# Performance work log

Hardware: AMD Instinct MI355X
Metric: run time of the kernel (lower is better)

The kernel has to match this reference:

```python
import jax, jax.numpy as jnp
import numpy as np

N = 2048  # device_num
K = 32    # neighbors per device


def setup_inputs() -> dict:
    key = jax.random.key(0)
    k1, k2, k3 = jax.random.split(key, 3)
    dynamic_re = jax.random.uniform(k1, (N, N), dtype=jnp.float32)
    static_re = jax.random.uniform(k2, (N,), dtype=jnp.float32)
    # neighbor ids in [0, N) excluding self (draw in [0, N-1) then shift past row index)
    r = jax.random.randint(k3, (N, K), 0, N - 1)
    rows = jnp.arange(N)[:, None]
    neighbor_matrix = (r + (r >= rows)).astype(jnp.int32)
    return {"dynamic_re": dynamic_re, "static_re": static_re, "neighbor_matrix": neighbor_matrix}


def _trust_forward(dynamic_re, static_re, neighbor_matrix):
    # Semantics of RobustTrustComputing.__call__ on a fresh instance (temp_storage empty):
    #  - diagonal: 1.0
    #  - neighbor (j in nbr(i)): history has len 1 -> CI branch is False -> combined
    #    tau = 0.7*dyn[i,j] + 0.3*stat[j]; prev==combined -> hysteresis takes the
    #    'x <= prev' path: sigmoid(combined + 0.5) with sigmoid(z)=(1-e^-z)/(1+e^-z)=tanh(z/2)
    #  - non-neighbor with common neighbors c: 0.8 * mean_c rep[i,c]*rep[c,j] read from the
    #    PARTIALLY-FILLED matrix in row-major write order (rep[i,c] nonzero only if c<j,
    #    rep[c,j] nonzero only if c<i); divisor is the FULL common-neighbor count.
    #  - non-neighbor, no common neighbors: 0.5*stat[j]
    #  - final clamp to [0,1]
    n = dynamic_re.shape[0]
    idx = jnp.arange(n)
    # membership matrix: M[i, c] True iff c appears in neighbor list of i
    M = jnp.zeros((n, n), dtype=bool).at[idx[:, None], neighbor_matrix].set(True)
    nbrval = jnp.tanh(0.5 * (0.7 * dynamic_re + 0.3 * static_re[None, :] + 0.5))
    Mf = M.astype(dynamic_re.dtype)
    count = Mf @ Mf.T                                  # |common neighbors(i, j)|
    Bmask = Mf.T * (idx[:, None] < idx[None, :])       # [c, j]: c in nbr(j) AND c < j
    fallback = 0.5 * static_re                         # [j]

    def step(rep, xs):
        i, M_i, nbr_i, cnt_i = xs
        # rep[i, c] (c in nbr(i)) equals nbrval[i, c] once column c has been written (c < j,
        # handled by Bmask); rep[c, j] is the final row c only for c < i (rows >= i are zero).
        A = jnp.where(M_i & (idx < i), nbr_i, 0.0)     # [c]
        num = jnp.einsum('c,cj,cj->j', A, rep, Bmask)  # [j]
        indirect = 0.8 * num / jnp.maximum(cnt_i, 1.0)
        row = jnp.where(M_i, nbr_i, jnp.where(cnt_i > 0, indirect, fallback))
        row = jnp.where(idx == i, 1.0, row)            # diagonal overrides everything
        return rep.at[i].set(row), None

    rep0 = jnp.zeros((n, n), dynamic_re.dtype)
    rep, _ = jax.lax.scan(step, rep0, (idx, M, nbrval, count))
    return jnp.clip(rep, 0.0, 1.0)


def reference(dynamic_re, static_re, neighbor_matrix):
    return _trust_forward(dynamic_re, static_re, neighbor_matrix)
```

## Files before the change

kernel.cpp:

```cpp
#include <hip/hip_runtime.h>
#include <math.h>
#include <limits.h>

#define WAVE 64
#define KMAX 32
#define IMAX 96

__device__ __forceinline__ float nvval(float d, float s) {
    float z = 0.7f * d + 0.3f * s + 0.5f;
    float e = __expf(z);
    return 1.0f - 2.0f / (e + 1.0f);
}
__device__ __forceinline__ float clamp01(float x) {
    return fminf(fmaxf(x, 0.0f), 1.0f);
}

__global__ void mbits_kernel(const int* __restrict__ nbr, int N, int K, int W,
                             unsigned* __restrict__ Mbits) {
    int tid = blockIdx.x * blockDim.x + threadIdx.x;
    int i = tid / WAVE;
    int lane = tid & (WAVE - 1);
    if (i >= N) return;
    int val = (lane < K) ? nbr[(size_t)i * K + lane] : INT_MAX;
    unsigned mybits = 0;
    #pragma unroll
    for (int t = 0; t < KMAX; ++t) {
        int vt = __shfl(val, t);
        if ((vt >> 5) == lane) mybits |= 1u << (vt & 31);
    }
    if (lane < W) Mbits[(size_t)i * W + lane] = mybits;
}

__global__ void __launch_bounds__(256) build_phase1(
        const float* __restrict__ dyn, const float* __restrict__ stat,
        const int* __restrict__ nbr, const unsigned* __restrict__ Mbits,
        int N, int K, int W,
        int* __restrict__ nbrs_sorted, int* __restrict__ invcnt,
        int* __restrict__ invlist, float* __restrict__ Vcomp,
        float* __restrict__ Dval) {
    __shared__ float s_nv[4 * KMAX * KMAX];
    int tid = blockIdx.x * blockDim.x + threadIdx.x;
    int j = tid / WAVE;
    int lane = threadIdx.x & (WAVE - 1);
    int waveid = threadIdx.x >> 6;
    if (j >= N) return;
    float* s_row = &s_nv[waveid * KMAX * KMAX];

    bool have = (lane < K);
    int val = have ? nbr[(size_t)j * K + lane] : INT_MAX;
    bool dup = false;
    #pragma unroll
    for (int t = 0; t < KMAX; ++t) {
        int vt = __shfl(val, t);
        if (have && t < lane && vt == val) dup = true;
    }
    int dupi = (dup || !have) ? 1 : 0;
    int pos = 0;
    #pragma unroll
    for (int t = 0; t < KMAX; ++t) {
        int vt = __shfl(val, t);
        int dt = __shfl(dupi, t);
        if (!dt && vt < val) pos++;
    }
    int myp = (have && !dup) ? pos : -1;
    int degj = __popcll(__ballot(have && !dup));

    int p = -1;
    if (have && !dup) {
        p = atomicAdd(&invcnt[val], 1);
        if (p >= 0 && p < IMAX) invlist[(size_t)val * IMAX + p] = j;
    }

    int c = INT_MAX;
    int psort = -1;
    #pragma unroll
    for (int t = 0; t < KMAX; ++t) {
        int pt = __shfl(myp, t);
        int vt = __shfl(val, t);
        int pp = __shfl(p, t);
        if (pt == lane) { c = vt; psort = pp; }
    }
    if (lane < K) nbrs_sorted[(size_t)j * K + lane] = c;
    bool validk = (lane < degj);
    float sk = validk ? stat[c] : 0.0f;
    float statj = stat[j];

    if (lane < K)
        Dval[(size_t)j * K + lane] = validk ? nvval(dyn[(size_t)j * N + c], sk) : 0.0f;

    unsigned dirbit = 0;
    if (validk) {
        unsigned w = Mbits[(size_t)c * W + (j >> 5)];
        dirbit = (w >> (j & 31)) & 1u;
    }
    unsigned dirmask = (unsigned)__ballot(dirbit != 0);
    float dv = 0.0f;
    if (dirbit) dv = nvval(dyn[(size_t)c * N + j], statj);

    unsigned hmAll = 0;
    #pragma unroll
    for (int m = 0; m < KMAX; ++m) {
        int cm = __shfl(c, m);
        if (cm < N) {
            unsigned w = validk ? Mbits[(size_t)cm * W + (c >> 5)] : 0u;
            unsigned b = (w >> (c & 31)) & 1u;
            hmAll |= b << m;
            if (b && lane < m && c < j)
                s_row[m * KMAX + lane] = nvval(dyn[(size_t)cm * N + c], sk);
        }
    }
    unsigned lm = (lane < 31) ? (0xFFFFFFFEu << lane) : 0u;
    unsigned hmTerm = (validk && c < j) ? (hmAll & lm) : 0u;

    int mycnt = 0;
    unsigned H = 0;
    #pragma unroll
    for (int m = 0; m < KMAX; ++m) {
        unsigned long long ball = __ballot((hmAll >> m) & 1u);
        unsigned long long ballT = __ballot((hmTerm >> m) & 1u);
        if (lane == m) mycnt = __popcll(ball);
        H |= (ballT ? 1u : 0u) << m;
    }
    H = __builtin_amdgcn_readfirstlane(H);
    dirmask = __builtin_amdgcn_readfirstlane(dirmask);

    float v = 0.0f;
    #pragma unroll
    for (int m = 0; m < KMAX; ++m) {
        float num = 0.0f;
        if (H & (1u << m)) {
            float t = 0.0f;
            if ((hmTerm >> m) & 1u) t = s_row[m * KMAX + lane] * v;
            num = t;
            num += __shfl_xor(num, 16);
            num += __shfl_xor(num, 8);
            num += __shfl_xor(num, 4);
            num += __shfl_xor(num, 2);
            num += __shfl_xor(num, 1);
        }
        float val2;
        if ((dirmask >> m) & 1u) val2 = dv;
        else if (mycnt > 0) val2 = 0.8f * num / (float)mycnt;
        else val2 = 0.5f * statj;
        val2 = clamp01(val2);
        if (lane == m) v = val2;
    }
    if (validk && psort >= 0 && psort < IMAX)
        Vcomp[(size_t)c * IMAX + psort] = v;
}

__global__ void __launch_bounds__(256) phase2(
        const float* __restrict__ stat,
        const int* __restrict__ nbrs_sorted,
        const int* __restrict__ invcnt, const int* __restrict__ invlist,
        const float* __restrict__ Vcomp, const float* __restrict__ Dval,
        int N, int K, float* __restrict__ out) {
    extern __shared__ char smem[];
    int* s_cnt = (int*)smem;
    float* s_num = (float*)(s_cnt + N);
    int* s_nbr = (int*)(s_num + N);
    float* s_nv = (float*)(s_nbr + KMAX);
    int* s_icnt = (int*)(s_nv + KMAX);
    __shared__ int s_me;

    int i = blockIdx.x;
    int tid = threadIdx.x;

    for (int t = tid; t < N; t += blockDim.x) { s_cnt[t] = 0; s_num[t] = 0.0f; }
    if (tid < K) {
        int c = nbrs_sorted[(size_t)i * K + tid];
        s_nbr[tid] = c;
        s_nv[tid] = Dval[(size_t)i * K + tid];
        int m = (c < N) ? invcnt[c] : 0;
        s_icnt[tid] = (m < 0) ? 0 : ((m < IMAX) ? m : IMAX);
    }
    if (tid == 0) {
        int m = invcnt[i];
        s_me = (m < 0) ? 0 : ((m < IMAX) ? m : IMAX);
    }
    __syncthreads();

    {
        int k = tid >> 3;
        int sub = tid & 7;
        if (k < K) {
            int c = s_nbr[k];
            int m = s_icnt[k];
            float nv = s_nv[k];
            if (c < N) {
                const int4* il4 = (const int4*)&invlist[(size_t)c * IMAX];
                const float4* vc4 = (const float4*)&Vcomp[(size_t)c * IMAX];
                for (int base = sub * 4; base < m; base += 32) {
                    int4 js = il4[base >> 2];
                    float4 vs = vc4[base >> 2];
                    int jj[4] = {js.x, js.y, js.z, js.w};
                    float vv[4] = {vs.x, vs.y, vs.z, vs.w};
                    #pragma unroll
                    for (int t = 0; t < 4; ++t) {
                        int e = base + t;
                        if (e < m) {
                            int j = jj[t] & (N - 1);
                            atomicAdd(&s_cnt[j], 1);
                            if (c < i && c < j)
                                atomicAdd(&s_num[j], nv * vv[t]);
                        }
                    }
                }
            }
        }
    }
    __syncthreads();

    if (tid < K) {
        int c = s_nbr[tid];
        if (c < N) { s_cnt[c] = -1; s_num[c] = s_nv[tid]; }
    }
    __syncthreads();

    int me = s_me;
    for (int e = tid; e < me; e += blockDim.x) {
        int j = invlist[(size_t)i * IMAX + e] & (N - 1);
        s_cnt[j] = -1;
        s_num[j] = Vcomp[(size_t)i * IMAX + e];
    }
    __syncthreads();

    for (int j = tid; j < N; j += blockDim.x) {
        int cnt = s_cnt[j];
        float val;
        if (j == i) val = 1.0f;
        else if (cnt < 0) val = s_num[j];
        else if (cnt > 0) val = 0.8f * s_num[j] / (float)cnt;
        else val = 0.5f * stat[j];
        out[(size_t)i * N + j] = clamp01(val);
    }
}

extern "C" void kernel_launch(void* const* d_in, const int* in_sizes, int n_in,
                              void* d_out, int out_size, void* d_ws, size_t ws_size,
                              hipStream_t stream) {
    const float* dyn = (const float*)d_in[0];
    const float* stat = (const float*)d_in[1];
    const int* nbr = (const int*)d_in[2];
    int N = in_sizes[1];
    int K = in_sizes[2] / N;
    int W = (N + 31) / 32;
    float* out = (float*)d_out;

    char* ws = (char*)d_ws;
    size_t offIC = 0;
    size_t offM = offIC + (size_t)N * sizeof(int);
    size_t offIL = offM + (size_t)N * W * sizeof(unsigned);
    size_t offVC = offIL + (size_t)N * IMAX * sizeof(int);
    size_t offNbr = offVC + (size_t)N * IMAX * sizeof(float);
    size_t offDv = offNbr + (size_t)N * K * sizeof(int);
    int* invcnt = (int*)(ws + offIC);
    unsigned* Mbits = (unsigned*)(ws + offM);
    int* invlist = (int*)(ws + offIL);
    float* Vcomp = (float*)(ws + offVC);
    int* nbrs_sorted = (int*)(ws + offNbr);
    float* Dval = (float*)(ws + offDv);

    hipMemsetAsync(ws + offIC, 0, (size_t)N * sizeof(int), stream);

    int threads = 256;
    int blocksWave = (N * WAVE + threads - 1) / threads;
    mbits_kernel<<<blocksWave, threads, 0, stream>>>(nbr, N, K, W, Mbits);
    build_phase1<<<blocksWave, threads, 0, stream>>>(dyn, stat, nbr, Mbits, N, K, W,
                                                     nbrs_sorted, invcnt, invlist,
                                                     Vcomp, Dval);
    size_t smem = (size_t)N * 8 + (size_t)KMAX * 12 + 16;
    phase2<<<N, threads, smem, stream>>>(stat, nbrs_sorted, invcnt, invlist,
                                         Vcomp, Dval, N, K, out);
}
```

Measured before the change: 115.1 us.

## Derive sorted neighbor lists from membership bitmap and split pair checks across half-waves

Drops the hipMemsetAsync by zeroing invcnt inside mbits_kernel. Builds each row's sorted, deduplicated neighbor list from the Mbits bitmap with a wave prefix scan instead of the O(K^2) shuffle-based dedup and rank. The pairwise membership loop now handles two m values per iteration, one per half-wave, which halves its trip count. This removes a launch and shuffle work, but it relies on the bitmap row fitting in 64 lanes (W<=64) and adds a data-dependent loop over set bits.

```diff
diff --git a/kernel.cpp b/kernel.cpp
--- a/kernel.cpp
+++ b/kernel.cpp
@@ -16,8 +16,9 @@
 }
 
 __global__ void mbits_kernel(const int* __restrict__ nbr, int N, int K, int W,
-                             unsigned* __restrict__ Mbits) {
+                             unsigned* __restrict__ Mbits, int* __restrict__ invcnt) {
     int tid = blockIdx.x * blockDim.x + threadIdx.x;
+    if (tid < N) invcnt[tid] = 0;
     int i = tid / WAVE;
     int lane = tid & (WAVE - 1);
     if (i >= N) return;
@@ -33,63 +34,63 @@
 
 __global__ void __launch_bounds__(256) build_phase1(
         const float* __restrict__ dyn, const float* __restrict__ stat,
-        const int* __restrict__ nbr, const unsigned* __restrict__ Mbits,
+        const unsigned* __restrict__ Mbits,
         int N, int K, int W,
         int* __restrict__ nbrs_sorted, int* __restrict__ invcnt,
         int* __restrict__ invlist, float* __restrict__ Vcomp,
         float* __restrict__ Dval) {
     __shared__ float s_nv[4 * KMAX * KMAX];
+    __shared__ int s_sortedAll[4 * KMAX];
     int tid = blockIdx.x * blockDim.x + threadIdx.x;
     int j = tid / WAVE;
     int lane = threadIdx.x & (WAVE - 1);
+    int l = lane & 31;
+    int half = lane >> 5;
     int waveid = threadIdx.x >> 6;
     if (j >= N) return;
     float* s_row = &s_nv[waveid * KMAX * KMAX];
-
-    bool have = (lane < K);
-    int val = have ? nbr[(size_t)j * K + lane] : INT_MAX;
-    bool dup = false;
-    #pragma unroll
-    for (int t = 0; t < KMAX; ++t) {
-        int vt = __shfl(val, t);
-        if (have && t < lane && vt == val) dup = true;
-    }
-    int dupi = (dup || !have) ? 1 : 0;
-    int pos = 0;
-    #pragma unroll
-    for (int t = 0; t < KMAX; ++t) {
-        int vt = __shfl(val, t);
-        int dt = __shfl(dupi, t);
-        if (!dt && vt < val) pos++;
-    }
-    int myp = (have && !dup) ? pos : -1;
-    int degj = __popcll(__ballot(have && !dup));
-
-    int p = -1;
-    if (have && !dup) {
-        p = atomicAdd(&invcnt[val], 1);
-        if (p >= 0 && p < IMAX) invlist[(size_t)val * IMAX + p] = j;
-    }
-
-    int c = INT_MAX;
+    int* s_sorted = &s_sortedAll[waveid * KMAX];
+
+    unsigned word = Mbits[(size_t)j * W + lane];
+    int myc = __popc(word);
+    int inc = myc;
+    #pragma unroll
+    for (int off = 1; off < 64; off <<= 1) {
+        int y = __shfl_up(inc, off);
+        if (lane >= off) inc += y;
+    }
+    int base = inc - myc;
+    int deg = __shfl(inc, 63);
+    {
+        unsigned wb = word;
+        int r = base;
+        while (wb) {
+            int b = __ffs(wb) - 1;
+            s_sorted[r] = (lane << 5) | b;
+            wb &= wb - 1;
+            ++r;
+        }
+    }
+    bool valid32 = (lane < deg);
+    int c = valid32 ? s_sorted[lane] : INT_MAX;
+    if (lane < K) nbrs_sorted[(size_t)j * K + lane] = c;
+
     int psort = -1;
-    #pragma unroll
-    for (int t = 0; t < KMAX; ++t) {
-        int pt = __shfl(myp, t);
-        int vt = __shfl(val, t);
-        int pp = __shfl(p, t);
-        if (pt == lane) { c = vt; psort = pp; }
-    }
-    if (lane < K) nbrs_sorted[(size_t)j * K + lane] = c;
-    bool validk = (lane < degj);
-    float sk = validk ? stat[c] : 0.0f;
+    if (valid32) {
+        psort = atomicAdd(&invcnt[c], 1);
+        if (psort >= 0 && psort < IMAX) invlist[(size_t)c * IMAX + psort] = j;
+    }
     float statj = stat[j];
+    float sk = valid32 ? stat[c] : 0.0f;
+    int c_m = __shfl(c, l);
+    float sk_m = __shfl(sk, l);
+    bool validl = (l < deg);
 
     if (lane < K)
-        Dval[(size_t)j * K + lane] = validk ? nvval(dyn[(size_t)j * N + c], sk) : 0.0f;
+        Dval[(size_t)j * K + lane] = valid32 ? nvval(dyn[(size_t)j * N + c], sk) : 0.0f;
 
     unsigned dirbit = 0;
-    if (validk) {
+    if (valid32) {
         unsigned w = Mbits[(size_t)c * W + (j >> 5)];
         dirbit = (w >> (j & 31)) & 1u;
     }
@@ -97,41 +98,44 @@
     float dv = 0.0f;
     if (dirbit) dv = nvval(dyn[(size_t)c * N + j], statj);
 
-    unsigned hmAll = 0;
-    #pragma unroll
-    for (int m = 0; m < KMAX; ++m) {
-        int cm = __shfl(c, m);
-        if (cm < N) {
-            unsigned w = validk ? Mbits[(size_t)cm * W + (c >> 5)] : 0u;
-            unsigned b = (w >> (c & 31)) & 1u;
-            hmAll |= b << m;
-            if (b && lane < m && c < j)
-                s_row[m * KMAX + lane] = nvval(dyn[(size_t)cm * N + c], sk);
-        }
-    }
-    unsigned lm = (lane < 31) ? (0xFFFFFFFEu << lane) : 0u;
-    unsigned hmTerm = (validk && c < j) ? (hmAll & lm) : 0u;
-
+    unsigned hmTerm = 0;
+    unsigned H = 0;
     int mycnt = 0;
-    unsigned H = 0;
-    #pragma unroll
-    for (int m = 0; m < KMAX; ++m) {
-        unsigned long long ball = __ballot((hmAll >> m) & 1u);
-        unsigned long long ballT = __ballot((hmTerm >> m) & 1u);
-        if (lane == m) mycnt = __popcll(ball);
-        H |= (ballT ? 1u : 0u) << m;
-    }
-    H = __builtin_amdgcn_readfirstlane(H);
-    dirmask = __builtin_amdgcn_readfirstlane(dirmask);
+    #pragma unroll
+    for (int t = 0; t < KMAX / 2; ++t) {
+        int mh = 2 * t + half;
+        int cm = __shfl(c, mh);
+        unsigned b = 0;
+        if (cm < N && validl) {
+            unsigned w = Mbits[(size_t)cm * W + (c_m >> 5)];
+            b = (w >> (c_m & 31)) & 1u;
+        }
+        bool termb = (b != 0) && (l < mh) && (c_m < j);
+        unsigned long long ball = __ballot(b != 0);
+        unsigned long long ballT = __ballot(termb);
+        unsigned low = (unsigned)ball;
+        unsigned high = (unsigned)(ball >> 32);
+        unsigned lowT = (unsigned)ballT;
+        unsigned highT = (unsigned)(ballT >> 32);
+        if (lane == 2 * t) mycnt = __popc(low);
+        if (lane == 2 * t + 1) mycnt = __popc(high);
+        hmTerm |= ((lowT >> l) & 1u) << (2 * t);
+        hmTerm |= ((highT >> l) & 1u) << (2 * t + 1);
+        H |= (lowT ? 1u : 0u) << (2 * t);
+        H |= (highT ? 1u : 0u) << (2 * t + 1);
+        if (termb)
+            s_row[mh * KMAX + l] = nvval(dyn[(size_t)cm * N + c_m], sk_m);
+    }
+    if (lane >= 32) hmTerm = 0;
 
     float v = 0.0f;
     #pragma unroll
     for (int m = 0; m < KMAX; ++m) {
         float num = 0.0f;
         if (H & (1u << m)) {
-            float t = 0.0f;
-            if ((hmTerm >> m) & 1u) t = s_row[m * KMAX + lane] * v;
-            num = t;
+            float tt = 0.0f;
+            if ((hmTerm >> m) & 1u) tt = s_row[m * KMAX + lane] * v;
+            num = tt;
             num += __shfl_xor(num, 16);
             num += __shfl_xor(num, 8);
             num += __shfl_xor(num, 4);
@@ -145,7 +149,7 @@
         val2 = clamp01(val2);
         if (lane == m) v = val2;
     }
-    if (validk && psort >= 0 && psort < IMAX)
+    if (valid32 && psort >= 0 && psort < IMAX)
         Vcomp[(size_t)c * IMAX + psort] = v;
 }
 
@@ -261,12 +265,10 @@
     int* nbrs_sorted = (int*)(ws + offNbr);
     float* Dval = (float*)(ws + offDv);
 
-    hipMemsetAsync(ws + offIC, 0, (size_t)N * sizeof(int), stream);
-
     int threads = 256;
     int blocksWave = (N * WAVE + threads - 1) / threads;
-    mbits_kernel<<<blocksWave, threads, 0, stream>>>(nbr, N, K, W, Mbits);
-    build_phase1<<<blocksWave, threads, 0, stream>>>(dyn, stat, nbr, Mbits, N, K, W,
+    mbits_kernel<<<blocksWave, threads, 0, stream>>>(nbr, N, K, W, Mbits, invcnt);
+    build_phase1<<<blocksWave, threads, 0, stream>>>(dyn, stat, Mbits, N, K, W,
                                                      nbrs_sorted, invcnt, invlist,
                                                      Vcomp, Dval);
     size_t smem = (size_t)N * 8 + (size_t)KMAX * 12 + 16;
```

Result: faster. 108.2 us (-6.0%).
